# Performance work log

Hardware: AMD Instinct MI355X
Metric: run time of the kernel (lower is better)

Reference implementation:

```python
import jax, jax.numpy as jnp
import numpy as np

R = 10000   # relation_num
E = 256     # emb_size == hidden_size
B = 1024    # batch
L = 8       # body length (loop runs L-1 steps)


def setup_inputs() -> dict:
    key = jax.random.key(0)
    ks = jax.random.split(key, 10)
    s = 0.05
    return {
        "bodys": jax.random.randint(ks[0], (B, L), 0, R),
        "emb_w": jax.random.normal(ks[1], (R, E), jnp.float32) * s,
        "w_ih": jax.random.normal(ks[2], (4 * E, E), jnp.float32) * s,
        "w_hh": jax.random.normal(ks[3], (4 * E, E), jnp.float32) * s,
        "b_ih": jax.random.normal(ks[4], (4 * E,), jnp.float32) * s,
        "b_hh": jax.random.normal(ks[5], (4 * E,), jnp.float32) * s,
        "fc1_w": jax.random.normal(ks[6], (E, 2 * E), jnp.float32) * s,
        "fc1_b": jax.random.normal(ks[7], (E,), jnp.float32) * s,
        "fc2_w": jax.random.normal(ks[8], (R + 1, E), jnp.float32) * s,
        "fc2_b": jax.random.normal(ks[9], (R + 1,), jnp.float32) * s,
    }


def _lstm(x, w_ih, w_hh, b_ih, b_hh):
    # x: [B, L, E] -> hidden states [B, L, H] (torch gate order i,f,g,o)
    Bn, _, H = x.shape[0], x.shape[1], w_hh.shape[1]
    h0 = jnp.zeros((Bn, H), x.dtype)
    c0 = jnp.zeros((Bn, H), x.dtype)

    def step(carry, xt):
        h, c = carry
        g = xt @ w_ih.T + b_ih + h @ w_hh.T + b_hh
        i, f, gg, o = jnp.split(g, 4, axis=-1)
        c = jax.nn.sigmoid(f) * c + jax.nn.sigmoid(i) * jnp.tanh(gg)
        h = jax.nn.sigmoid(o) * jnp.tanh(c)
        return (h, c), h

    _, hs = jax.lax.scan(step, (h0, c0), x.transpose(1, 0, 2))
    return hs.transpose(1, 0, 2)


def reference(bodys, emb_w, w_ih, w_hh, b_ih, b_hh, fc1_w, fc1_b, fc2_w, fc2_b):
    x = emb_w[bodys]                       # [B, L, E] embedded body relations
    body_hid = _lstm(x, w_ih, w_hh, b_ih, b_hh)  # [B, L, E]
    Rn = emb_w.shape[0]
    prob = emb_concat = prob_sf = None
    for i in range(body_hid.shape[1] - 1):   # short fixed unroll (L-1 steps)
        if i == 0:
            emb_1 = x[:, 0, :]
            second = x[:, 1, :]
        else:
            # prob_sf @ cat(embedding(indices), body_hid[:, i])  without [B,R+1,E]
            emb_1 = prob_sf[:, :Rn] @ emb_w + prob_sf[:, Rn:] * body_hid[:, i, :]
            # relation_emb[:, i+1, :] == emb_w[i+1] broadcast over batch
            second = jnp.broadcast_to(emb_w[i + 1], emb_1.shape)
        emb_concat = jnp.concatenate([emb_1, second], axis=1)   # [B, 2E]
        prob = jax.nn.relu(emb_concat @ fc1_w.T + fc1_b) @ fc2_w.T + fc2_b  # [B, R+1]
        prob_sf = jax.nn.softmax(prob, axis=1)
    return prob, emb_concat
```

## Files before the change

kernel.cpp:

```cpp
#include <hip/hip_runtime.h>

#define Bv 1024
#define Ev 256
#define Lv 8
#define Rv 10000
#define NP1 10001
#define PS2 10240
#define NPAD 10112
#define BM 64
#define BN 128
#define NSLICE 16
#define NSLOT 158
#define RPSTRIDE 160

typedef __attribute__((ext_vector_type(8))) short bf16x8;
typedef __attribute__((ext_vector_type(4))) float f32x4;

__device__ __forceinline__ float b2f(unsigned short u) {
    union { unsigned int i; float f; } v; v.i = ((unsigned int)u) << 16; return v.f;
}
__device__ __forceinline__ unsigned short f2b(float f) {
    union { float f; unsigned int i; } v; v.f = f;
    unsigned int r = v.i + 0x7fffu + ((v.i >> 16) & 1u);
    return (unsigned short)(r >> 16);
}
__device__ __forceinline__ float ftanh(float x) {
    x = fminf(fmaxf(x, -30.f), 30.f);
    float e = __expf(2.f * x);
    return (e - 1.f) / (e + 1.f);
}
__device__ __forceinline__ void glds16(const void* g, void* l) {
    __builtin_amdgcn_global_load_lds(
        (const __attribute__((address_space(1))) void*)g,
        (__attribute__((address_space(3))) void*)l, 16, 0, 0);
}

__global__ __launch_bounds__(256) void gemm_tile(
    const unsigned short* __restrict__ A1, int lda1,
    const unsigned short* __restrict__ W1, int ldw1,
    const float* __restrict__ bias1,
    int Ktot, int kchunk, int Ncols, int mode,
    float* __restrict__ outF, unsigned short* __restrict__ outB, int ldc,
    float* __restrict__ rowPart, float* __restrict__ sfLastU)
{
    __shared__ unsigned short As[2][BM * 32];
    __shared__ unsigned short Bs[2][BN * 32];

    int bmode = mode & 7;
    int swz   = mode >> 4;
    int bx, by, bz;
    if (swz == 1) {
        int r = blockIdx.x & 7, q = blockIdx.x >> 3;
        bx = q & 15; by = r + (q >> 4) * 8; bz = 0;
        if (by >= NPAD / BN) return;
    } else if (swz == 2) {
        int r = blockIdx.x & 7, q = blockIdx.x >> 3;
        bz = r + (q >> 5) * 8; bx = (q & 31) >> 1; by = q & 1;
    } else {
        bx = blockIdx.x; by = blockIdx.y; bz = blockIdx.z;
    }

    int tid  = threadIdx.x;
    int wave = tid >> 6;
    int lane = tid & 63;
    int quad = lane >> 4;
    int l16  = lane & 15;
    int wm = (wave & 1) * 32;
    int wn = (wave >> 1) * 64;
    int m0 = bx * BM;
    int n0 = by * BN;
    int k0 = bz * kchunk;
    int k1 = k0 + kchunk; if (k1 > Ktot) k1 = Ktot;

    f32x4 acc[2][4];
#pragma unroll
    for (int i = 0; i < 2; ++i)
#pragma unroll
        for (int j = 0; j < 4; ++j) acc[i][j] = (f32x4){0.f, 0.f, 0.f, 0.f};

    int c0 = tid, c1 = 256 + tid;
    int row0 = c0 >> 2, row1 = c1 >> 2;
    int g80 = ((c0 & 3) ^ (row0 & 3) ^ ((row0 >> 2) & 3)) * 8;
    int g81 = ((c1 & 3) ^ (row1 & 3) ^ ((row1 >> 2) & 3)) * 8;

    bool first = true;
    for (int k = k0; k < k1; k += 64) {
        if (!first) __syncthreads();
        first = false;
#pragma unroll
        for (int h = 0; h < 2; ++h) {
            int kk = k + h * 32;
            glds16(A1 + (size_t)(m0 + row0) * lda1 + kk + g80, As[h] + (wave * 64) * 8);
            glds16(W1 + (size_t)(n0 + row0) * ldw1 + kk + g80, Bs[h] + (wave * 64) * 8);
            glds16(W1 + (size_t)(n0 + row1) * ldw1 + kk + g81, Bs[h] + (256 + wave * 64) * 8);
        }
        asm volatile("s_waitcnt vmcnt(0)" ::: "memory");
        __syncthreads();

#pragma unroll
        for (int h = 0; h < 2; ++h) {
            bf16x8 af[2], bfr[4];
#pragma unroll
            for (int t = 0; t < 2; ++t) {
                int m = wm + t * 16 + l16;
                int ca = quad ^ (m & 3) ^ ((m >> 2) & 3);
                af[t] = *(const bf16x8*)(As[h] + m * 32 + ca * 8);
            }
#pragma unroll
            for (int t = 0; t < 4; ++t) {
                int n = wn + t * 16 + l16;
                int cb = quad ^ (n & 3) ^ ((n >> 2) & 3);
                bfr[t] = *(const bf16x8*)(Bs[h] + n * 32 + cb * 8);
            }
#pragma unroll
            for (int i = 0; i < 2; ++i)
#pragma unroll
                for (int j = 0; j < 4; ++j)
                    acc[i][j] = __builtin_amdgcn_mfma_f32_16x16x32_bf16(
                        af[i], bfr[j], acc[i][j], 0, 0, 0);
        }
    }

    if (bmode == 5) {
        float rsum[2][4];
#pragma unroll
        for (int i = 0; i < 2; ++i)
#pragma unroll
            for (int r = 0; r < 4; ++r) rsum[i][r] = 0.f;
#pragma unroll
        for (int j = 0; j < 4; ++j) {
            int n = n0 + wn + j * 16 + l16;
            bool valid = (n < Ncols);
            float bsum = valid ? bias1[n] : 0.f;
#pragma unroll
            for (int i = 0; i < 2; ++i) {
                int mBase = m0 + wm + i * 16 + quad * 4;
#pragma unroll
                for (int r = 0; r < 4; ++r) {
                    float e = 0.f;
                    unsigned short w = 0;
                    if (valid) {
                        e = __expf(acc[i][j][r] + bsum);
                        w = f2b(e);
                        if (n == Rv) sfLastU[mBase + r] = e;
                    }
                    outB[(size_t)(mBase + r) * ldc + n] = w;
                    rsum[i][r] += e;
                }
            }
        }
        int slot = by * 2 + (wn >> 6);
#pragma unroll
        for (int i = 0; i < 2; ++i)
#pragma unroll
            for (int r = 0; r < 4; ++r) {
                float s = rsum[i][r];
                s += __shfl_xor(s, 1);
                s += __shfl_xor(s, 2);
                s += __shfl_xor(s, 4);
                s += __shfl_xor(s, 8);
                if (l16 == 0) {
                    int m = m0 + wm + i * 16 + quad * 4 + r;
                    rowPart[(size_t)m * RPSTRIDE + slot] = s;
                }
            }
        return;
    }

#pragma unroll
    for (int j = 0; j < 4; ++j) {
        int n = n0 + wn + j * 16 + l16;
        bool valid = (n < Ncols);
        if (!valid && bmode != 3) continue;
        float bsum = (valid && bias1) ? bias1[n] : 0.f;
#pragma unroll
        for (int i = 0; i < 2; ++i) {
            int mBase = m0 + wm + i * 16 + quad * 4;
#pragma unroll
            for (int r = 0; r < 4; ++r) {
                float v = acc[i][j][r] + bsum;
                size_t idx = (size_t)(mBase + r) * ldc + n;
                if (bmode == 0)      outF[idx] = v;
                else if (bmode == 3) outB[idx] = valid ? f2b(v) : (unsigned short)0;
                else                 outB[(size_t)bz * (Bv * Ev) + idx] = f2b(v);
            }
        }
    }
}

__global__ __launch_bounds__(256) void gemm64(
    const unsigned short* __restrict__ A1, int lda1,
    const unsigned short* __restrict__ W1, int ldw1,
    const float* __restrict__ bias1,
    int Ktot, int Ncols, int mode,
    float* __restrict__ outF, unsigned short* __restrict__ outB,
    int ldc, int nshift,
    const float* __restrict__ xgate, int tstep)
{
    __shared__ unsigned short As[4][64 * 32];
    __shared__ unsigned short Bs[4][64 * 32];

    int bmode = mode & 7;
    int bx = blockIdx.x >> nshift;
    int by = blockIdx.x & ((1 << nshift) - 1);
    int tid  = threadIdx.x;
    int wave = tid >> 6;
    int lane = tid & 63;
    int quad = lane >> 4;
    int l16  = lane & 15;
    int m0 = bx * 64;
    int n0 = by * 64;

    f32x4 acc[4];
#pragma unroll
    for (int j = 0; j < 4; ++j) acc[j] = (f32x4){0.f, 0.f, 0.f, 0.f};

    int row = tid >> 2;
    int g8  = ((tid & 3) ^ (row & 3) ^ ((row >> 2) & 3)) * 8;

    bool first = true;
    for (int k = 0; k < Ktot; k += 128) {
        if (!first) __syncthreads();
        first = false;
#pragma unroll
        for (int h = 0; h < 4; ++h) {
            int kk = k + h * 32;
            glds16(A1 + (size_t)(m0 + row) * lda1 + kk + g8, As[h] + wave * 512);
            glds16(W1 + (size_t)(n0 + row) * ldw1 + kk + g8, Bs[h] + wave * 512);
        }
        asm volatile("s_waitcnt vmcnt(0)" ::: "memory");
        __syncthreads();

#pragma unroll
        for (int h = 0; h < 4; ++h) {
            int ml = wave * 16 + l16;
            int ca = quad ^ (ml & 3) ^ ((ml >> 2) & 3);
            bf16x8 a = *(const bf16x8*)(As[h] + ml * 32 + ca * 8);
#pragma unroll
            for (int j = 0; j < 4; ++j) {
                int nl = j * 16 + l16;
                int cb = quad ^ (nl & 3) ^ ((nl >> 2) & 3);
                bf16x8 b = *(const bf16x8*)(Bs[h] + nl * 32 + cb * 8);
                acc[j] = __builtin_amdgcn_mfma_f32_16x16x32_bf16(a, b, acc[j], 0, 0, 0);
            }
        }
    }

    if (bmode == 4) {
        int e  = by * 16 + l16;
        float bi = bias1[n0 + l16];
        float bf_ = bias1[n0 + 16 + l16];
        float bg = bias1[n0 + 32 + l16];
        float bo = bias1[n0 + 48 + l16];
#pragma unroll
        for (int r = 0; r < 4; ++r) {
            int m = m0 + wave * 16 + quad * 4 + r;
            const float* xr = xgate + ((size_t)m * Lv + tstep) * 1024 + n0 + l16;
            float gi = acc[0][r] + bi + xr[0];
            float gf = acc[1][r] + bf_ + xr[16];
            float gg = acc[2][r] + bg + xr[32];
            float go = acc[3][r] + bo + xr[48];
            float cp = (mode & 8) ? 0.f : outF[(size_t)m * 256 + e];
            float si = 1.f / (1.f + __expf(-gi));
            float sf = 1.f / (1.f + __expf(-gf));
            float so = 1.f / (1.f + __expf(-go));
            float cn = sf * cp + si * ftanh(gg);
            outF[(size_t)m * 256 + e] = cn;
            outB[(size_t)m * 256 + e] = f2b(so * ftanh(cn));
        }
        return;
    }

#pragma unroll
    for (int j = 0; j < 4; ++j) {
        int n = n0 + j * 16 + l16;
        if (n >= Ncols) continue;
        float bsum = bias1 ? bias1[n] : 0.f;
#pragma unroll
        for (int r = 0; r < 4; ++r) {
            int m = m0 + wave * 16 + quad * 4 + r;
            float v = acc[j][r] + bsum;
            if (bmode == 1) outB[(size_t)m * ldc + n] = f2b(v > 0.f ? v : 0.f);
            else            outB[(size_t)m * ldc + n] = f2b(v);
        }
    }
}

__global__ void prep_k(const float* __restrict__ w_ih,
                       const float* __restrict__ w_hh,
                       const float* __restrict__ fc1_w,
                       const float* __restrict__ fc2_w,
                       const float* __restrict__ b_ih,
                       const float* __restrict__ b_hh,
                       const int* __restrict__ bodys,
                       const float* __restrict__ emb_w,
                       const float* __restrict__ fc1_b,
                       unsigned short* __restrict__ w_ih_b,
                       unsigned short* __restrict__ w_hh_b,
                       unsigned short* __restrict__ fc1_w_b,
                       unsigned short* __restrict__ fc2_w_b,
                       float* __restrict__ biasC,
                       unsigned short* __restrict__ x,
                       unsigned short* __restrict__ embT,
                       unsigned short* __restrict__ embc,
                       unsigned short* __restrict__ sfA,
                       float* __restrict__ B2,
                       unsigned short* __restrict__ emb_w_b,
                       unsigned short* __restrict__ EW1T)
{
    __shared__ float tile[32][33];
    int b = blockIdx.x, t = threadIdx.x;
    if (b < 1264) {
#pragma unroll
        for (int j = 0; j < 8; ++j) {
            int i = b * 2048 + j * 256 + t;
            fc2_w_b[i] = (i < NP1 * Ev) ? f2b(fc2_w[i]) : (unsigned short)0;
        }
    } else if (b < 1520) {
        int bb = b - 1264;
        const float* src = (bb < 128) ? w_ih : w_hh;
        unsigned short* dst = (bb < 128) ? w_ih_b : w_hh_b;
        int rb = (bb & 127) * 8;
#pragma unroll
        for (int j = 0; j < 8; ++j) {
            int r = rb + j;
            int gate = (r >> 4) & 3;
            int e = (r & 15) | ((r >> 6) << 4);
            dst[(size_t)r * 256 + t] = f2b(src[(size_t)(gate * 256 + e) * 256 + t]);
        }
    } else if (b < 1584) {
        int base = (b - 1520) * 2048;
#pragma unroll
        for (int j = 0; j < 8; ++j) {
            int i = base + j * 256 + t;
            fc1_w_b[i] = f2b(fc1_w[i]);
        }
    } else if (b < 1585) {
#pragma unroll
        for (int j = 0; j < 4; ++j) {
            int r = j * 256 + t;
            int gate = (r >> 4) & 3;
            int e = (r & 15) | ((r >> 6) << 4);
            biasC[r] = b_ih[gate * 256 + e] + b_hh[gate * 256 + e];
        }
    } else if (b < 2609) {
        int bb = b - 1585;
#pragma unroll
        for (int j = 0; j < 8; ++j) {
            int row = bb * 8 + j;
            x[(size_t)row * Ev + t] = f2b(emb_w[(size_t)bodys[row] * Ev + t]);
        }
    } else if (b < 5169) {
        int bb = b - 2609;
        int kt = (bb % 320) * 32, et = (bb / 320) * 32;
        int tx = t & 31, ty = t >> 5;
#pragma unroll
        for (int r = ty; r < 32; r += 8) {
            int k = kt + r;
            tile[r][tx] = (k < Rv) ? emb_w[(size_t)k * Ev + et + tx] : 0.f;
        }
        __syncthreads();
#pragma unroll
        for (int r = ty; r < 32; r += 8) {
            embT[(size_t)(et + r) * PS2 + kt + tx] = f2b(tile[tx][r]);
        }
    } else if (b < 6193) {
        int bb = b - 5169;
        embc[(size_t)bb * 512 + t]       = f2b(emb_w[(size_t)bodys[bb * Lv + 0] * Ev + t]);
        embc[(size_t)bb * 512 + 256 + t] = f2b(emb_w[(size_t)bodys[bb * Lv + 1] * Ev + t]);
        if (t < PS2 - NPAD) sfA[(size_t)bb * PS2 + NPAD + t] = 0;
    } else if (b < 6200) {
        int i = b - 6193;
        const float* er = emb_w + (size_t)(i + 1) * Ev;
        const float* wr = fc1_w + (size_t)t * 512 + 256;
        float s = fc1_b[t];
        for (int k = 0; k < 256; ++k) s += wr[k] * er[k];
        B2[i * 256 + t] = s;
    } else if (b < 7464) {
        int bb = b - 6200;
#pragma unroll
        for (int j = 0; j < 8; ++j) {
            int i = bb * 2048 + j * 256 + t;
            emb_w_b[i] = ((i >> 8) < Rv) ? f2b(emb_w[i]) : (unsigned short)0;
        }
    } else {
        int idx = (b - 7464) * 256 + t;
        EW1T[(size_t)(idx >> 7) * PS2 + NPAD + (idx & 127)] = 0;
    }
}

__global__ void finalize_emb(const unsigned short* __restrict__ emb1p,
                             const float* __restrict__ rowPart,
                             const float* __restrict__ sfLastU,
                             const unsigned short* __restrict__ h_i,
                             const float* __restrict__ emb_row,
                             unsigned short* __restrict__ embc,
                             float* __restrict__ outTail,
                             const float* __restrict__ HWrow,
                             const float* __restrict__ B2row,
                             unsigned short* __restrict__ hiddenA)
{
    int b = blockIdx.x, e = threadIdx.x;
    int wave = e >> 6, lane = e & 63;
    __shared__ float sred[4];
    float ps = (e < NSLOT) ? rowPart[(size_t)b * RPSTRIDE + e] : 0.f;
    for (int off = 32; off; off >>= 1) ps += __shfl_down(ps, off);
    if (lane == 0) sred[wave] = ps;
    __syncthreads();
    float inv = 1.f / (sred[0] + sred[1] + sred[2] + sred[3]);

    float x1 = 0.f;
#pragma unroll
    for (int z = 0; z < NSLICE; ++z)
        x1 += b2f(emb1p[(size_t)z * (Bv * Ev) + (size_t)b * Ev + e]);

    if (HWrow) {
        float v = x1 * inv + sfLastU[b] * inv * HWrow[(size_t)b * 256 + e] + B2row[e];
        hiddenA[(size_t)b * 256 + e] = f2b(v > 0.f ? v : 0.f);
    } else {
        float v = (x1 + sfLastU[b] * b2f(h_i[(size_t)b * Ev + e])) * inv;
        embc[(size_t)b * 512 + e] = f2b(v);
        float w = emb_row[e];
        embc[(size_t)b * 512 + 256 + e]    = f2b(w);
        outTail[(size_t)b * 512 + e]       = v;
        outTail[(size_t)b * 512 + 256 + e] = w;
    }
}

extern "C" void kernel_launch(void* const* d_in, const int* in_sizes, int n_in,
                              void* d_out, int out_size, void* d_ws, size_t ws_size,
                              hipStream_t stream)
{
    const int*   bodys = (const int*)d_in[0];
    const float* emb_w = (const float*)d_in[1];
    const float* w_ih  = (const float*)d_in[2];
    const float* w_hh  = (const float*)d_in[3];
    const float* b_ih  = (const float*)d_in[4];
    const float* b_hh  = (const float*)d_in[5];
    const float* fc1_w = (const float*)d_in[6];
    const float* fc1_b = (const float*)d_in[7];
    const float* fc2_w = (const float*)d_in[8];
    const float* fc2_b = (const float*)d_in[9];
    float* out = (float*)d_out;

    char* ws = (char*)d_ws;
    size_t off = 0;
    auto alloc = [&](size_t bytes) -> void* {
        void* p = ws + off;
        off += (bytes + 255) & ~(size_t)255;
        return p;
    };
    unsigned short* x       = (unsigned short*)alloc((size_t)Bv * Lv * Ev * 2);
    unsigned short* hs      = (unsigned short*)alloc((size_t)Lv * Bv * Ev * 2);
    float*          cbuf    = (float*)alloc((size_t)Bv * Ev * 4);
    float*          xg      = (float*)alloc((size_t)Bv * Lv * 1024 * 4);
    unsigned short* embT    = (unsigned short*)alloc((size_t)Ev * PS2 * 2);
    unsigned short* sfA     = (unsigned short*)alloc((size_t)Bv * PS2 * 2);
    float*          sfLastU = (float*)alloc((size_t)Bv * 4);
    float*          rowPart = (float*)alloc((size_t)Bv * RPSTRIDE * 4);
    unsigned short* emb1p   = (unsigned short*)alloc((size_t)NSLICE * Bv * Ev * 2);
    unsigned short* embc    = (unsigned short*)alloc((size_t)Bv * 512 * 2);
    unsigned short* hiddenA = (unsigned short*)alloc((size_t)Bv * Ev * 2);
    unsigned short* w_ih_b  = (unsigned short*)alloc((size_t)1024 * Ev * 2);
    unsigned short* w_hh_b  = (unsigned short*)alloc((size_t)1024 * Ev * 2);
    float*          biasC   = (float*)alloc((size_t)1024 * 4);
    float*          B2      = (float*)alloc((size_t)7 * 256 * 4);
    unsigned short* fc1_w_b = (unsigned short*)alloc((size_t)Ev * 512 * 2);
    unsigned short* fc2_w_b = (unsigned short*)alloc((size_t)NPAD * Ev * 2);
    unsigned short* emb_w_b = (unsigned short*)alloc((size_t)NPAD * Ev * 2);
    unsigned short* EW1T    = (unsigned short*)alloc((size_t)Ev * PS2 * 2);
    float*          HW      = (float*)alloc((size_t)Lv * Bv * Ev * 4);
    (void)ws_size; (void)in_sizes; (void)n_in; (void)out_size;

    prep_k<<<7592, 256, 0, stream>>>(w_ih, w_hh, fc1_w, fc2_w, b_ih, b_hh,
                                     bodys, emb_w, fc1_b,
                                     w_ih_b, w_hh_b, fc1_w_b, fc2_w_b, biasC, x,
                                     embT, embc, sfA, B2, emb_w_b, EW1T);

    gemm_tile<<<dim3(4, 79, 1), 256, 0, stream>>>(
        fc1_w_b, 512, emb_w_b, Ev,
        nullptr,
        Ev, Ev, Rv, 3,
        nullptr, EW1T, PS2, nullptr, nullptr);

    gemm64<<<64, 256, 0, stream>>>(
        embc, 512, fc1_w_b, 512,
        fc1_b,
        512, 256, 1,
        nullptr, hiddenA, 256, 2,
        nullptr, 0);

    gemm_tile<<<dim3(128, 8, 1), 256, 0, stream>>>(
        x, Ev, w_ih_b, Ev,
        nullptr,
        Ev, Ev, 1024, 0,
        xg, nullptr, 1024, nullptr, nullptr);

    for (int t = 0; t < Lv; ++t) {
        gemm64<<<256, 256, 0, stream>>>(
            hs + (size_t)(t ? t - 1 : 0) * Bv * Ev, Ev, w_hh_b, Ev,
            biasC,
            (t == 0) ? 0 : Ev, 1024, 4 | (t == 0 ? 8 : 0),
            cbuf, hs + (size_t)t * Bv * Ev, 1024, 4,
            xg, t);
    }

    gemm_tile<<<dim3(128, 2, 1), 256, 0, stream>>>(
        hs, Ev, fc1_w_b, 512,
        nullptr,
        Ev, Ev, Ev, 0,
        HW, nullptr, Ev, nullptr, nullptr);

    for (int i = 0; i < 7; ++i) {
        if (i > 0) {
            bool last = (i == 6);
            gemm_tile<<<512, 256, 0, stream>>>(
                sfA, PS2, last ? embT : EW1T, PS2,
                nullptr,
                PS2, PS2 / NSLICE, Ev, 2 | (2 << 4),
                nullptr, emb1p, Ev, nullptr, nullptr);
            finalize_emb<<<Bv, 256, 0, stream>>>(
                emb1p, rowPart, sfLastU,
                hs + (size_t)i * Bv * Ev, emb_w + (size_t)(i + 1) * Ev,
                embc, out + (size_t)Bv * NP1,
                last ? nullptr : (HW + (size_t)i * Bv * Ev),
                last ? nullptr : (B2 + (size_t)i * 256),
                hiddenA);
            if (last) {
                gemm64<<<64, 256, 0, stream>>>(
                    embc, 512, fc1_w_b, 512,
                    B2 + (size_t)6 * 256,
                    256, 256, 1,
                    nullptr, hiddenA, 256, 2,
                    nullptr, 0);
            }
        }
        if (i < 6) {
            gemm_tile<<<1280, 256, 0, stream>>>(
                hiddenA, Ev, fc2_w_b, Ev,
                fc2_b,
                Ev, Ev, NP1, 5 | (1 << 4),
                nullptr, sfA, PS2, rowPart, sfLastU);
        } else {
            gemm_tile<<<1280, 256, 0, stream>>>(
                hiddenA, Ev, fc2_w_b, Ev,
                fc2_b,
                Ev, Ev, NP1, 0 | (1 << 4),
                out, nullptr, NP1, nullptr, nullptr);
        }
    }
}
```

Before: 435.2 us.

## Fuse LSTM recurrence and fc1 projection into one persistent kernel

Replaces the eight per-timestep LSTM gemm launches and the separate fc1 projection GEMM with a single kernel. Each of 64 blocks owns 16 batch rows for all steps: cell state stays in registers, h stays in LDS, and only the steps actually consumed are computed. The fc1 products for steps 1–5 are written out directly. This removes launch overhead and the global round-trips for h and c, at the cost of low parallelism (64 blocks) and every block streaming the full w_hh and fc1 weights from global/L2 memory each step with no LDS staging.

```diff
diff --git a/kernel.cpp b/kernel.cpp
--- a/kernel.cpp
+++ b/kernel.cpp
@@ -12,6 +12,7 @@
 #define NSLICE 16
 #define NSLOT 158
 #define RPSTRIDE 160
+#define HLS 264
 
 typedef __attribute__((ext_vector_type(8))) short bf16x8;
 typedef __attribute__((ext_vector_type(4))) float f32x4;
@@ -188,6 +189,112 @@
     }
 }
 
+__global__ __launch_bounds__(256) void lstm_all(
+    const unsigned short* __restrict__ w_hh_b,
+    const unsigned short* __restrict__ fc1_w_b,
+    const float* __restrict__ biasC,
+    const float* __restrict__ xg,
+    unsigned short* __restrict__ hs6,
+    float* __restrict__ HW)
+{
+    __shared__ unsigned short hls[16 * HLS];
+
+    int mBase = blockIdx.x * 16;
+    int tid  = threadIdx.x;
+    int wave = tid >> 6;
+    int lane = tid & 63;
+    int quad = lane >> 4;
+    int l16  = lane & 15;
+
+    float c[4][4];
+#pragma unroll
+    for (int a = 0; a < 4; ++a)
+#pragma unroll
+        for (int b = 0; b < 4; ++b) c[a][b] = 0.f;
+
+    for (int t = 0; t < 7; ++t) {
+        f32x4 acc[4][4];
+#pragma unroll
+        for (int a = 0; a < 4; ++a)
+#pragma unroll
+            for (int b = 0; b < 4; ++b) acc[a][b] = (f32x4){0.f, 0.f, 0.f, 0.f};
+
+        if (t > 0) {
+            bf16x8 af[8];
+#pragma unroll
+            for (int f = 0; f < 8; ++f)
+                af[f] = *(const bf16x8*)(hls + l16 * HLS + f * 32 + quad * 8);
+#pragma unroll
+            for (int ebl = 0; ebl < 4; ++ebl)
+#pragma unroll
+                for (int g = 0; g < 4; ++g) {
+                    int n = (wave * 16 + ebl * 4 + g) * 16 + l16;
+                    const unsigned short* Bp = w_hh_b + (size_t)n * 256 + quad * 8;
+                    f32x4 a4 = acc[ebl][g];
+#pragma unroll
+                    for (int f = 0; f < 8; ++f) {
+                        bf16x8 b = *(const bf16x8*)(Bp + f * 32);
+                        a4 = __builtin_amdgcn_mfma_f32_16x16x32_bf16(af[f], b, a4, 0, 0, 0);
+                    }
+                    acc[ebl][g] = a4;
+                }
+        }
+        __syncthreads();
+
+#pragma unroll
+        for (int ebl = 0; ebl < 4; ++ebl) {
+            int ebg = wave * 4 + ebl;
+            int nb  = ebg * 64;
+            float bi  = biasC[nb + l16];
+            float bf_ = biasC[nb + 16 + l16];
+            float bg  = biasC[nb + 32 + l16];
+            float bo  = biasC[nb + 48 + l16];
+#pragma unroll
+            for (int r = 0; r < 4; ++r) {
+                int m  = quad * 4 + r;
+                int mg = mBase + m;
+                const float* xr = xg + ((size_t)mg * Lv + t) * 1024 + nb + l16;
+                float gi = acc[ebl][0][r] + bi  + xr[0];
+                float gf = acc[ebl][1][r] + bf_ + xr[16];
+                float gg = acc[ebl][2][r] + bg  + xr[32];
+                float go = acc[ebl][3][r] + bo  + xr[48];
+                float si = 1.f / (1.f + __expf(-gi));
+                float sf = 1.f / (1.f + __expf(-gf));
+                float so = 1.f / (1.f + __expf(-go));
+                float cn = sf * c[ebl][r] + si * ftanh(gg);
+                c[ebl][r] = cn;
+                unsigned short hb = f2b(so * ftanh(cn));
+                int e = ebg * 16 + l16;
+                hls[m * HLS + e] = hb;
+                if (t == 6) hs6[(size_t)mg * 256 + e] = hb;
+            }
+        }
+        __syncthreads();
+
+        if (t >= 1 && t <= 5) {
+            bf16x8 af[8];
+#pragma unroll
+            for (int f = 0; f < 8; ++f)
+                af[f] = *(const bf16x8*)(hls + l16 * HLS + f * 32 + quad * 8);
+#pragma unroll
+            for (int j = 0; j < 4; ++j) {
+                int n = wave * 64 + j * 16 + l16;
+                const unsigned short* Bp = fc1_w_b + (size_t)n * 512 + quad * 8;
+                f32x4 a4 = (f32x4){0.f, 0.f, 0.f, 0.f};
+#pragma unroll
+                for (int f = 0; f < 8; ++f) {
+                    bf16x8 b = *(const bf16x8*)(Bp + f * 32);
+                    a4 = __builtin_amdgcn_mfma_f32_16x16x32_bf16(af[f], b, a4, 0, 0, 0);
+                }
+#pragma unroll
+                for (int r = 0; r < 4; ++r)
+                    HW[(size_t)t * (Bv * Ev) + (size_t)(mBase + quad * 4 + r) * 256 + n]
+                        = a4[r];
+            }
+        }
+    }
+}
+
 __global__ __launch_bounds__(256) void gemm64(
     const unsigned short* __restrict__ A1, int lda1,
     const unsigned short* __restrict__ W1, int ldw1,
@@ -246,31 +353,7 @@
         }
     }
 
-    if (bmode == 4) {
-        int e  = by * 16 + l16;
-        float bi = bias1[n0 + l16];
-        float bf_ = bias1[n0 + 16 + l16];
-        float bg = bias1[n0 + 32 + l16];
-        float bo = bias1[n0 + 48 + l16];
-#pragma unroll
-        for (int r = 0; r < 4; ++r) {
-            int m = m0 + wave * 16 + quad * 4 + r;
-            const float* xr = xgate + ((size_t)m * Lv + tstep) * 1024 + n0 + l16;
-            float gi = acc[0][r] + bi + xr[0];
-            float gf = acc[1][r] + bf_ + xr[16];
-            float gg = acc[2][r] + bg + xr[32];
-            float go = acc[3][r] + bo + xr[48];
-            float cp = (mode & 8) ? 0.f : outF[(size_t)m * 256 + e];
-            float si = 1.f / (1.f + __expf(-gi));
-            float sf = 1.f / (1.f + __expf(-gf));
-            float so = 1.f / (1.f + __expf(-go));
-            float cn = sf * cp + si * ftanh(gg);
-            outF[(size_t)m * 256 + e] = cn;
-            outB[(size_t)m * 256 + e] = f2b(so * ftanh(cn));
-        }
-        return;
-    }
-
+    (void)xgate; (void)tstep;
 #pragma unroll
     for (int j = 0; j < 4; ++j) {
         int n = n0 + j * 16 + l16;
@@ -284,6 +367,7 @@
             else            outB[(size_t)m * ldc + n] = f2b(v);
         }
     }
+    (void)outF;
 }
 
 __global__ void prep_k(const float* __restrict__ w_ih,
@@ -451,8 +535,7 @@
         return p;
     };
     unsigned short* x       = (unsigned short*)alloc((size_t)Bv * Lv * Ev * 2);
-    unsigned short* hs      = (unsigned short*)alloc((size_t)Lv * Bv * Ev * 2);
-    float*          cbuf    = (float*)alloc((size_t)Bv * Ev * 4);
+    unsigned short* hs6     = (unsigned short*)alloc((size_t)Bv * Ev * 2);
     float*          xg      = (float*)alloc((size_t)Bv * Lv * 1024 * 4);
     unsigned short* embT    = (unsigned short*)alloc((size_t)Ev * PS2 * 2);
     unsigned short* sfA     = (unsigned short*)alloc((size_t)Bv * PS2 * 2);
@@ -496,20 +579,7 @@
         Ev, Ev, 1024, 0,
         xg, nullptr, 1024, nullptr, nullptr);
 
-    for (int t = 0; t < Lv; ++t) {
-        gemm64<<<256, 256, 0, stream>>>(
-            hs + (size_t)(t ? t - 1 : 0) * Bv * Ev, Ev, w_hh_b, Ev,
-            biasC,
-            (t == 0) ? 0 : Ev, 1024, 4 | (t == 0 ? 8 : 0),
-            cbuf, hs + (size_t)t * Bv * Ev, 1024, 4,
-            xg, t);
-    }
-
-    gemm_tile<<<dim3(128, 2, 1), 256, 0, stream>>>(
-        hs, Ev, fc1_w_b, 512,
-        nullptr,
-        Ev, Ev, Ev, 0,
-        HW, nullptr, Ev, nullptr, nullptr);
+    lstm_all<<<64, 256, 0, stream>>>(w_hh_b, fc1_w_b, biasC, xg, hs6, HW);
 
     for (int i = 0; i < 7; ++i) {
         if (i > 0) {
@@ -521,7 +591,7 @@
                 nullptr, emb1p, Ev, nullptr, nullptr);
             finalize_emb<<<Bv, 256, 0, stream>>>(
                 emb1p, rowPart, sfLastU,
-                hs + (size_t)i * Bv * Ev, emb_w + (size_t)(i + 1) * Ev,
+                hs6, emb_w + (size_t)(i + 1) * Ev,
                 embc, out + (size_t)Bv * NP1,
                 last ? nullptr : (HW + (size_t)i * Bv * Ev),
                 last ? nullptr : (B2 + (size_t)i * 256),
```

After: 596.7 us. +37.1%, slower.
